# Performance work log

Hardware: AMD Instinct MI355X
Metric: run time of the kernel (lower is better)

## Reference

```python
import jax, jax.numpy as jnp
import numpy as np

N = 8192  # number of nodes
F = 8     # feature dim


def setup_inputs() -> dict:
    key = jax.random.key(0)
    ks = jax.random.split(key, 24)
    inp = {
        "adj": jax.random.uniform(ks[0], (N, N), jnp.float32),
        "dist_from_prev": jax.random.uniform(ks[1], (N,), jnp.float32),
        "dist_to_start": jax.random.uniform(ks[2], (N,), jnp.float32),
    }
    dims = {"l0": (2, F), "l1": (F, F), "pol": (F, 1), "val": (F, 1)}
    i = 3
    for name, (din, dout) in dims.items():
        inp[f"W1_{name}"] = jax.random.normal(ks[i], (din, dout), jnp.float32) * 0.3; i += 1
        inp[f"b1_{name}"] = jax.random.normal(ks[i], (dout,), jnp.float32) * 0.1; i += 1
        inp[f"W2_{name}"] = jax.random.normal(ks[i], (dout, dout), jnp.float32) * 0.3; i += 1
        inp[f"b2_{name}"] = jax.random.normal(ks[i], (dout,), jnp.float32) * 0.1; i += 1
    return inp


def _mlp(x, adj, W1, b1, W2, b2):
    # GIN-style layer: aggregate then 2-layer MLP
    h = adj @ x                     # [N, din] aggregation (memory bound)
    h = jax.nn.relu(h @ W1 + b1)    # [N, dout]
    return h @ W2 + b2              # [N, dout]


def reference(adj, dist_from_prev, dist_to_start,
              W1_l0, b1_l0, W2_l0, b2_l0,
              W1_l1, b1_l1, W2_l1, b2_l1,
              W1_pol, b1_pol, W2_pol, b2_pol,
              W1_val, b1_val, W2_val, b2_val):
    cur = jnp.stack([dist_from_prev, dist_to_start], axis=1)  # [N, 2]
    # hidden GIN layers + relu (dropout is identity in eval mode)
    cur = jax.nn.relu(_mlp(cur, adj, W1_l0, b1_l0, W2_l0, b2_l0))
    cur = jax.nn.relu(_mlp(cur, adj, W1_l1, b1_l1, W2_l1, b2_l1))
    policy = jax.nn.softmax(_mlp(cur, adj, W1_pol, b1_pol, W2_pol, b2_pol)[:, 0], axis=0)  # [N]
    value = _mlp(cur, adj, W1_val, b1_val, W2_val, b2_val)[:, 0]  # [N]
    m = value.mean()
    std = jnp.sqrt(jnp.mean((value - m) ** 2) + 1e-10)
    normalized_value = (value - m) / std
    return policy, normalized_value
```

## Files before the change

kernel.cpp:

```cpp
#include <hip/hip_runtime.h>
#include <math.h>

#define NN 8192
typedef unsigned int u32;

__device__ __forceinline__ u32 dot4u(u32 a, u32 b, u32 c) {
#if __has_builtin(__builtin_amdgcn_udot4)
  return __builtin_amdgcn_udot4(a, b, c, false);
#else
  c += (a & 0xffu) * (b & 0xffu);
  c += ((a >> 8) & 0xffu) * ((b >> 8) & 0xffu);
  c += ((a >> 16) & 0xffu) * ((b >> 16) & 0xffu);
  c += (a >> 24) * (b >> 24);
  return c;
#endif
}

__global__ __launch_bounds__(256, 8) void pass1_kernel(
    const float* __restrict__ adj, u32* __restrict__ adj8,
    const float* __restrict__ dfp, const float* __restrict__ dts,
    const float* __restrict__ W1, const float* __restrict__ b1,
    const float* __restrict__ W2, const float* __restrict__ b2,
    float* __restrict__ cur, float* __restrict__ partial,
    u32* __restrict__ cnt) {
  const int tid = threadIdx.x, wave = tid >> 6, lane = tid & 63;
  const int row = blockIdx.x * 4 + wave;
  __shared__ float wmax[4][8];
  if (blockIdx.x == 0 && tid == 0) cnt[0] = 0;

  const float* rowp = adj + (size_t)row * NN;
  u32* qp = adj8 + (size_t)row * 2048;

  float acc0 = 0.f, acc1 = 0.f;
  float4 A0 = *(const float4*)(rowp + 4 * lane);
  float4 A1 = *(const float4*)(rowp + 256 + 4 * lane);
  for (int c = 0; c < 16; ++c) {
    const int kb = 512 * c;
    float4 xp0 = *(const float4*)(dfp + kb + 4 * lane);
    float4 xp1 = *(const float4*)(dfp + kb + 256 + 4 * lane);
    float4 xs0 = *(const float4*)(dts + kb + 4 * lane);
    float4 xs1 = *(const float4*)(dts + kb + 256 + 4 * lane);
    float4 B0, B1;
    if (c < 15) {
      B0 = *(const float4*)(rowp + kb + 512 + 4 * lane);
      B1 = *(const float4*)(rowp + kb + 768 + 4 * lane);
    } else {
      B0 = A0; B1 = A1;
    }
    acc0 = fmaf(A0.x, xp0.x, acc0); acc0 = fmaf(A0.y, xp0.y, acc0);
    acc0 = fmaf(A0.z, xp0.z, acc0); acc0 = fmaf(A0.w, xp0.w, acc0);
    acc0 = fmaf(A1.x, xp1.x, acc0); acc0 = fmaf(A1.y, xp1.y, acc0);
    acc0 = fmaf(A1.z, xp1.z, acc0); acc0 = fmaf(A1.w, xp1.w, acc0);
    acc1 = fmaf(A0.x, xs0.x, acc1); acc1 = fmaf(A0.y, xs0.y, acc1);
    acc1 = fmaf(A0.z, xs0.z, acc1); acc1 = fmaf(A0.w, xs0.w, acc1);
    acc1 = fmaf(A1.x, xs1.x, acc1); acc1 = fmaf(A1.y, xs1.y, acc1);
    acc1 = fmaf(A1.z, xs1.z, acc1); acc1 = fmaf(A1.w, xs1.w, acc1);
    {
      u32 q0 = (u32)fmaf(A0.x, 255.f, 0.5f);
      u32 q1 = (u32)fmaf(A0.y, 255.f, 0.5f);
      u32 q2 = (u32)fmaf(A0.z, 255.f, 0.5f);
      u32 q3 = (u32)fmaf(A0.w, 255.f, 0.5f);
      qp[128 * c + lane] = q0 | (q1 << 8) | (q2 << 16) | (q3 << 24);
      q0 = (u32)fmaf(A1.x, 255.f, 0.5f);
      q1 = (u32)fmaf(A1.y, 255.f, 0.5f);
      q2 = (u32)fmaf(A1.z, 255.f, 0.5f);
      q3 = (u32)fmaf(A1.w, 255.f, 0.5f);
      qp[128 * c + 64 + lane] = q0 | (q1 << 8) | (q2 << 16) | (q3 << 24);
    }
    A0 = B0; A1 = B1;
  }
  for (int off = 32; off; off >>= 1) {
    acc0 += __shfl_xor(acc0, off, 64);
    acc1 += __shfl_xor(acc1, off, 64);
  }
  const int j = lane & 7;
  float z = fmaf(acc0, W1[j], fmaf(acc1, W1[8 + j], b1[j]));
  z = fmaxf(z, 0.f);
  float o = b2[j];
#pragma unroll
  for (int jj = 0; jj < 8; ++jj)
    o = fmaf(__shfl(z, jj, 64), W2[jj * 8 + j], o);
  float val = fmaxf(o, 0.f);
  if (lane < 8) {
    cur[(size_t)row * 8 + j] = val;
    wmax[wave][j] = val;
  }
  __syncthreads();
  if (tid < 8)
    partial[blockIdx.x * 8 + tid] = fmaxf(fmaxf(wmax[0][tid], wmax[1][tid]),
                                          fmaxf(wmax[2][tid], wmax[3][tid]));
}

template <int HEADS>
__global__ __launch_bounds__(512, 4) void pass23_kernel(
    const u32* __restrict__ adj8, const float* __restrict__ x,
    const float* __restrict__ partial, int nprod,
    const float* __restrict__ W1, const float* __restrict__ b1,
    const float* __restrict__ W2, const float* __restrict__ b2,
    const float* __restrict__ W1v, const float* __restrict__ b1v,
    const float* __restrict__ W2v, const float* __restrict__ b2v,
    float* __restrict__ out0, float* __restrict__ out1,
    float* __restrict__ partial_out, u32* __restrict__ cnt) {
  __shared__ u32 sxT[8 * 2048];
  __shared__ float redM[8][8];
  __shared__ float sqs[8], sds[8];
  __shared__ float wmax[8][8];
  __shared__ float sa[8], sb[8], sc[4];
  __shared__ int lastFlag;
  const int tid = threadIdx.x, wave = tid >> 6, lane = tid & 63;
  const int row0 = blockIdx.x * 16 + wave * 2;

  const u32* r0p = adj8 + (size_t)row0 * 2048;
  const u32* r1p = adj8 + (size_t)(row0 + 1) * 2048;
  uint4 A[2], Bp[2];
  A[0] = *(const uint4*)(r0p + 4 * lane);
  A[1] = *(const uint4*)(r1p + 4 * lane);
  Bp[0] = *(const uint4*)(r0p + 256 + 4 * lane);
  Bp[1] = *(const uint4*)(r1p + 256 + 4 * lane);

  float pm[8] = {0.f, 0.f, 0.f, 0.f, 0.f, 0.f, 0.f, 0.f};
  for (int p = tid; p < nprod; p += 512) {
    float4 a = *(const float4*)(partial + p * 8);
    float4 b = *(const float4*)(partial + p * 8 + 4);
    pm[0] = fmaxf(pm[0], a.x); pm[1] = fmaxf(pm[1], a.y);
    pm[2] = fmaxf(pm[2], a.z); pm[3] = fmaxf(pm[3], a.w);
    pm[4] = fmaxf(pm[4], b.x); pm[5] = fmaxf(pm[5], b.y);
    pm[6] = fmaxf(pm[6], b.z); pm[7] = fmaxf(pm[7], b.w);
  }
  for (int off = 32; off; off >>= 1)
#pragma unroll
    for (int j = 0; j < 8; ++j) pm[j] = fmaxf(pm[j], __shfl_xor(pm[j], off, 64));
  if (lane == 0)
#pragma unroll
    for (int j = 0; j < 8; ++j) redM[wave][j] = pm[j];
  __syncthreads();
  if (tid < 8) {
    float m2 = 0.f;
#pragma unroll
    for (int w = 0; w < 8; ++w) m2 = fmaxf(m2, redM[w][tid]);
    m2 = fmaxf(m2, 1e-20f);
    sqs[tid] = 255.f / m2;
    sds[tid] = m2 / 65025.f;
  }
  __syncthreads();

  float qs[8];
#pragma unroll
  for (int j = 0; j < 8; ++j) qs[j] = sqs[j];
  for (int gi = 0; gi < 4; ++gi) {
    const int p = gi * 512 + tid;
    u32 pk[8] = {0, 0, 0, 0, 0, 0, 0, 0};
#pragma unroll
    for (int m = 0; m < 4; ++m) {
      const float* xr = x + (size_t)(4 * p + m) * 8;
      float4 a = *(const float4*)xr;
      float4 b = *(const float4*)(xr + 4);
      const float e[8] = {a.x, a.y, a.z, a.w, b.x, b.y, b.z, b.w};
#pragma unroll
      for (int j = 0; j < 8; ++j)
        pk[j] |= ((u32)fmaf(e[j], qs[j], 0.5f)) << (8 * m);
    }
#pragma unroll
    for (int j = 0; j < 8; ++j) sxT[j * 2048 + p] = pk[j];
  }
  __syncthreads();

  u32 acc[2][8] = {};
  for (int c = 0; c < 8; ++c) {
    uint4 C[2];
    if (c + 2 < 8) {
      C[0] = *(const uint4*)(r0p + 256 * (c + 2) + 4 * lane);
      C[1] = *(const uint4*)(r1p + 256 * (c + 2) + 4 * lane);
    } else {
      C[0] = A[0];
      C[1] = A[1];
    }
    uint4 xq[8];
#pragma unroll
    for (int jj = 0; jj < 8; ++jj)
      xq[jj] = ((const uint4*)sxT)[jj * 512 + 64 * c + lane];
#pragma unroll
    for (int r = 0; r < 2; ++r) {
      const uint4 a4 = A[r];
#pragma unroll
      for (int jj = 0; jj < 8; ++jj) {
        u32 cc = acc[r][jj];
        cc = dot4u(a4.x, xq[jj].x, cc);
        cc = dot4u(a4.y, xq[jj].y, cc);
        cc = dot4u(a4.z, xq[jj].z, cc);
        cc = dot4u(a4.w, xq[jj].w, cc);
        acc[r][jj] = cc;
      }
    }
    A[0] = Bp[0]; A[1] = Bp[1];
    Bp[0] = C[0]; Bp[1] = C[1];
  }
#pragma unroll
  for (int r = 0; r < 2; ++r)
#pragma unroll
    for (int jj = 0; jj < 8; ++jj)
      for (int off = 32; off; off >>= 1)
        acc[r][jj] += (u32)__shfl_xor((int)acc[r][jj], off, 64);
  float h[2][8];
#pragma unroll
  for (int r = 0; r < 2; ++r)
#pragma unroll
    for (int jj = 0; jj < 8; ++jj) h[r][jj] = (float)acc[r][jj] * sds[jj];

  if (HEADS == 0) {
    const int j = lane & 7;
    float mxv = 0.f;
#pragma unroll
    for (int r = 0; r < 2; ++r) {
      float z = b1[j];
#pragma unroll
      for (int d = 0; d < 8; ++d) z = fmaf(h[r][d], W1[d * 8 + j], z);
      z = fmaxf(z, 0.f);
      float o = b2[j];
#pragma unroll
      for (int jj = 0; jj < 8; ++jj)
        o = fmaf(__shfl(z, jj, 64), W2[jj * 8 + j], o);
      float val = fmaxf(o, 0.f);
      if (lane < 8) out0[(size_t)(row0 + r) * 8 + j] = val;
      mxv = fmaxf(mxv, val);
    }
    if (lane < 8) wmax[wave][lane] = mxv;
    __syncthreads();
    if (tid < 8) {
      float m2 = 0.f;
#pragma unroll
      for (int w = 0; w < 8; ++w) m2 = fmaxf(m2, wmax[w][tid]);
      partial_out[blockIdx.x * 8 + tid] = m2;
    }
  } else {
    if (lane == 0) {
#pragma unroll
      for (int r = 0; r < 2; ++r) {
        float zp = b1[0], zv = b1v[0];
#pragma unroll
        for (int d = 0; d < 8; ++d) {
          zp = fmaf(h[r][d], W1[d], zp);
          zv = fmaf(h[r][d], W1v[d], zv);
        }
        zp = fmaxf(zp, 0.f);
        zv = fmaxf(zv, 0.f);
        out0[row0 + r] = fmaf(zp, W2[0], b2[0]);
        out1[row0 + r] = fmaf(zv, W2v[0], b2v[0]);
      }
    }
    __syncthreads();
    if (tid == 0) {
      __threadfence();
      u32 old = atomicAdd(cnt, 1);
      lastFlag = (old == (u32)(gridDim.x - 1)) ? 1 : 0;
    }
    __syncthreads();
    if (lastFlag) {
      __threadfence();
      float lv[16], vv[16];
#pragma unroll
      for (int i = 0; i < 4; ++i) {
        float4 a = *(const float4*)(out0 + tid * 16 + 4 * i);
        float4 b = *(const float4*)(out1 + tid * 16 + 4 * i);
        lv[4 * i] = a.x; lv[4 * i + 1] = a.y; lv[4 * i + 2] = a.z; lv[4 * i + 3] = a.w;
        vv[4 * i] = b.x; vv[4 * i + 1] = b.y; vv[4 * i + 2] = b.z; vv[4 * i + 3] = b.w;
      }
      float m = -3.4e38f, s = 0.f;
#pragma unroll
      for (int i = 0; i < 16; ++i) {
        m = fmaxf(m, lv[i]);
        s += vv[i];
      }
      for (int off = 32; off; off >>= 1) {
        m = fmaxf(m, __shfl_xor(m, off, 64));
        s += __shfl_xor(s, off, 64);
      }
      if (lane == 0) { sa[wave] = m; sb[wave] = s; }
      __syncthreads();
      if (tid == 0) {
        float mm = sa[0], ss = sb[0];
        for (int i = 1; i < 8; ++i) { mm = fmaxf(mm, sa[i]); ss += sb[i]; }
        sc[0] = mm; sc[1] = ss * (1.f / NN);
      }
      __syncthreads();
      m = sc[0];
      const float mean = sc[1];
      float e = 0.f, v2 = 0.f;
#pragma unroll
      for (int i = 0; i < 16; ++i) {
        e += expf(lv[i] - m);
        float d = vv[i] - mean;
        v2 = fmaf(d, d, v2);
      }
      for (int off = 32; off; off >>= 1) {
        e += __shfl_xor(e, off, 64);
        v2 += __shfl_xor(v2, off, 64);
      }
      if (lane == 0) { sa[wave] = e; sb[wave] = v2; }
      __syncthreads();
      if (tid == 0) {
        float ee = sa[0], vvv = sb[0];
        for (int i = 1; i < 8; ++i) { ee += sa[i]; vvv += sb[i]; }
        sc[2] = 1.f / ee;
        sc[3] = 1.f / sqrtf(vvv * (1.f / NN) + 1e-10f);
      }
      __syncthreads();
      const float inv_e = sc[2], inv_std = sc[3];
#pragma unroll
      for (int i = 0; i < 4; ++i) {
        float4 po, nv;
        po.x = expf(lv[4 * i] - m) * inv_e;
        po.y = expf(lv[4 * i + 1] - m) * inv_e;
        po.z = expf(lv[4 * i + 2] - m) * inv_e;
        po.w = expf(lv[4 * i + 3] - m) * inv_e;
        nv.x = (vv[4 * i] - mean) * inv_std;
        nv.y = (vv[4 * i + 1] - mean) * inv_std;
        nv.z = (vv[4 * i + 2] - mean) * inv_std;
        nv.w = (vv[4 * i + 3] - mean) * inv_std;
        *(float4*)(out0 + tid * 16 + 4 * i) = po;
        *(float4*)(out1 + tid * 16 + 4 * i) = nv;
      }
    }
  }
}

extern "C" void kernel_launch(void* const* d_in, const int* in_sizes, int n_in,
                              void* d_out, int out_size, void* d_ws,
                              size_t ws_size, hipStream_t stream) {
  const float* adj = (const float*)d_in[0];
  const float* dfp = (const float*)d_in[1];
  const float* dts = (const float*)d_in[2];
  const float* W1_l0 = (const float*)d_in[3];
  const float* b1_l0 = (const float*)d_in[4];
  const float* W2_l0 = (const float*)d_in[5];
  const float* b2_l0 = (const float*)d_in[6];
  const float* W1_l1 = (const float*)d_in[7];
  const float* b1_l1 = (const float*)d_in[8];
  const float* W2_l1 = (const float*)d_in[9];
  const float* b2_l1 = (const float*)d_in[10];
  const float* W1_pol = (const float*)d_in[11];
  const float* b1_pol = (const float*)d_in[12];
  const float* W2_pol = (const float*)d_in[13];
  const float* b2_pol = (const float*)d_in[14];
  const float* W1_val = (const float*)d_in[15];
  const float* b1_val = (const float*)d_in[16];
  const float* W2_val = (const float*)d_in[17];
  const float* b2_val = (const float*)d_in[18];

  char* base = (char*)d_ws;
  u32* adj8 = (u32*)base;
  float* curA = (float*)(base + (size_t)NN * NN);
  float* curB = curA + NN * 8;
  float* partialA = curB + NN * 8;
  float* partialB = partialA + 2048 * 8;
  u32* cnt = (u32*)(partialB + 512 * 8);
  float* logits = (float*)d_out;
  float* value = logits + NN;

  pass1_kernel<<<2048, 256, 0, stream>>>(adj, adj8, dfp, dts, W1_l0, b1_l0,
                                         W2_l0, b2_l0, curA, partialA, cnt);
  pass23_kernel<0><<<512, 512, 0, stream>>>(
      adj8, curA, partialA, 2048, W1_l1, b1_l1, W2_l1, b2_l1, W1_l1, b1_l1,
      W2_l1, b2_l1, curB, curB, partialB, cnt);
  pass23_kernel<1><<<512, 512, 0, stream>>>(
      adj8, curB, partialB, 512, W1_pol, b1_pol, W2_pol, b2_pol, W1_val,
      b1_val, W2_val, b2_val, logits, value, partialB, cnt);
}
```

Baseline: 151.4 us.

## Split quantization into streaming kernel and run layer-0 aggregation on uint8 adjacency

The fused first pass is split in two. A grid-stride kernel now only converts the fp32 adjacency to packed uint8, and a new layer-0 kernel reads that uint8 copy and does the aggregation with udot4 against quantized input features. The aim is a leaner streaming quantization pass and an integer aggregation that matches the later passes. In exchange it adds an extra 64 MB read of adj8 and one more launch, and quantizing the distance features to 8 bits adds numeric error.

```diff
diff --git a/kernel.cpp b/kernel.cpp
--- a/kernel.cpp
+++ b/kernel.cpp
@@ -16,79 +16,117 @@
 #endif
 }
 
-__global__ __launch_bounds__(256, 8) void pass1_kernel(
-    const float* __restrict__ adj, u32* __restrict__ adj8,
-    const float* __restrict__ dfp, const float* __restrict__ dts,
-    const float* __restrict__ W1, const float* __restrict__ b1,
-    const float* __restrict__ W2, const float* __restrict__ b2,
-    float* __restrict__ cur, float* __restrict__ partial,
+__device__ __forceinline__ u32 pack255(float4 v) {
+  u32 q0 = (u32)fmaf(v.x, 255.f, 0.5f);
+  u32 q1 = (u32)fmaf(v.y, 255.f, 0.5f);
+  u32 q2 = (u32)fmaf(v.z, 255.f, 0.5f);
+  u32 q3 = (u32)fmaf(v.w, 255.f, 0.5f);
+  return q0 | (q1 << 8) | (q2 << 16) | (q3 << 24);
+}
+
+__global__ __launch_bounds__(256) void quant_kernel(
+    const float4* __restrict__ adj4, u32* __restrict__ adj8,
     u32* __restrict__ cnt) {
+  if (blockIdx.x == 0 && threadIdx.x == 0) cnt[0] = 0;
+  const size_t n4 = (size_t)NN * NN / 4;
+  const size_t stride = (size_t)gridDim.x * 256;
+  for (size_t i = (size_t)blockIdx.x * 256 + threadIdx.x; i < n4;
+       i += 4 * stride) {
+    float4 v0 = adj4[i];
+    float4 v1 = adj4[i + stride];
+    float4 v2 = adj4[i + 2 * stride];
+    float4 v3 = adj4[i + 3 * stride];
+    adj8[i] = pack255(v0);
+    adj8[i + stride] = pack255(v1);
+    adj8[i + 2 * stride] = pack255(v2);
+    adj8[i + 3 * stride] = pack255(v3);
+  }
+}
+
+__global__ __launch_bounds__(512, 4) void agg0_kernel(
+    const u32* __restrict__ adj8, const float* __restrict__ dfp,
+    const float* __restrict__ dts, const float* __restrict__ W1,
+    const float* __restrict__ b1, const float* __restrict__ W2,
+    const float* __restrict__ b2, float* __restrict__ cur,
+    float* __restrict__ partial) {
+  __shared__ u32 sxT[2 * 2048];
+  __shared__ float wmax[8][8];
   const int tid = threadIdx.x, wave = tid >> 6, lane = tid & 63;
-  const int row = blockIdx.x * 4 + wave;
-  __shared__ float wmax[4][8];
-  if (blockIdx.x == 0 && tid == 0) cnt[0] = 0;
-
-  const float* rowp = adj + (size_t)row * NN;
-  u32* qp = adj8 + (size_t)row * 2048;
-
-  float acc0 = 0.f, acc1 = 0.f;
-  float4 A0 = *(const float4*)(rowp + 4 * lane);
-  float4 A1 = *(const float4*)(rowp + 256 + 4 * lane);
-  for (int c = 0; c < 16; ++c) {
-    const int kb = 512 * c;
-    float4 xp0 = *(const float4*)(dfp + kb + 4 * lane);
-    float4 xp1 = *(const float4*)(dfp + kb + 256 + 4 * lane);
-    float4 xs0 = *(const float4*)(dts + kb + 4 * lane);
-    float4 xs1 = *(const float4*)(dts + kb + 256 + 4 * lane);
-    float4 B0, B1;
-    if (c < 15) {
-      B0 = *(const float4*)(rowp + kb + 512 + 4 * lane);
-      B1 = *(const float4*)(rowp + kb + 768 + 4 * lane);
+  const int row0 = blockIdx.x * 16 + wave * 2;
+  const u32* r0p = adj8 + (size_t)row0 * 2048;
+  const u32* r1p = adj8 + (size_t)(row0 + 1) * 2048;
+
+  uint4 A[2], Bp[2];
+  A[0] = *(const uint4*)(r0p + 4 * lane);
+  A[1] = *(const uint4*)(r1p + 4 * lane);
+  Bp[0] = *(const uint4*)(r0p + 256 + 4 * lane);
+  Bp[1] = *(const uint4*)(r1p + 256 + 4 * lane);
+
+  for (int gi = 0; gi < 4; ++gi) {
+    const int p = gi * 512 + tid;
+    float4 a = *(const float4*)(dfp + 4 * p);
+    float4 b = *(const float4*)(dts + 4 * p);
+    sxT[p] = pack255(a);
+    sxT[2048 + p] = pack255(b);
+  }
+  __syncthreads();
+
+  u32 acc[2][2] = {};
+  for (int c = 0; c < 8; ++c) {
+    uint4 C[2];
+    if (c + 2 < 8) {
+      C[0] = *(const uint4*)(r0p + 256 * (c + 2) + 4 * lane);
+      C[1] = *(const uint4*)(r1p + 256 * (c + 2) + 4 * lane);
     } else {
-      B0 = A0; B1 = A1;
-    }
-    acc0 = fmaf(A0.x, xp0.x, acc0); acc0 = fmaf(A0.y, xp0.y, acc0);
-    acc0 = fmaf(A0.z, xp0.z, acc0); acc0 = fmaf(A0.w, xp0.w, acc0);
-    acc0 = fmaf(A1.x, xp1.x, acc0); acc0 = fmaf(A1.y, xp1.y, acc0);
-    acc0 = fmaf(A1.z, xp1.z, acc0); acc0 = fmaf(A1.w, xp1.w, acc0);
-    acc1 = fmaf(A0.x, xs0.x, acc1); acc1 = fmaf(A0.y, xs0.y, acc1);
-    acc1 = fmaf(A0.z, xs0.z, acc1); acc1 = fmaf(A0.w, xs0.w, acc1);
-    acc1 = fmaf(A1.x, xs1.x, acc1); acc1 = fmaf(A1.y, xs1.y, acc1);
-    acc1 = fmaf(A1.z, xs1.z, acc1); acc1 = fmaf(A1.w, xs1.w, acc1);
-    {
-      u32 q0 = (u32)fmaf(A0.x, 255.f, 0.5f);
-      u32 q1 = (u32)fmaf(A0.y, 255.f, 0.5f);
-      u32 q2 = (u32)fmaf(A0.z, 255.f, 0.5f);
-      u32 q3 = (u32)fmaf(A0.w, 255.f, 0.5f);
-      qp[128 * c + lane] = q0 | (q1 << 8) | (q2 << 16) | (q3 << 24);
-      q0 = (u32)fmaf(A1.x, 255.f, 0.5f);
-      q1 = (u32)fmaf(A1.y, 255.f, 0.5f);
-      q2 = (u32)fmaf(A1.z, 255.f, 0.5f);
-      q3 = (u32)fmaf(A1.w, 255.f, 0.5f);
-      qp[128 * c + 64 + lane] = q0 | (q1 << 8) | (q2 << 16) | (q3 << 24);
-    }
-    A0 = B0; A1 = B1;
-  }
-  for (int off = 32; off; off >>= 1) {
-    acc0 += __shfl_xor(acc0, off, 64);
-    acc1 += __shfl_xor(acc1, off, 64);
-  }
+      C[0] = A[0];
+      C[1] = A[1];
+    }
+    uint4 x0 = ((const uint4*)sxT)[64 * c + lane];
+    uint4 x1 = ((const uint4*)sxT)[512 + 64 * c + lane];
+#pragma unroll
+    for (int r = 0; r < 2; ++r) {
+      const uint4 a4 = A[r];
+      u32 c0 = acc[r][0], c1 = acc[r][1];
+      c0 = dot4u(a4.x, x0.x, c0); c0 = dot4u(a4.y, x0.y, c0);
+      c0 = dot4u(a4.z, x0.z, c0); c0 = dot4u(a4.w, x0.w, c0);
+      c1 = dot4u(a4.x, x1.x, c1); c1 = dot4u(a4.y, x1.y, c1);
+      c1 = dot4u(a4.z, x1.z, c1); c1 = dot4u(a4.w, x1.w, c1);
+      acc[r][0] = c0; acc[r][1] = c1;
+    }
+    A[0] = Bp[0]; A[1] = Bp[1];
+    Bp[0] = C[0]; Bp[1] = C[1];
+  }
+#pragma unroll
+  for (int r = 0; r < 2; ++r)
+#pragma unroll
+    for (int f = 0; f < 2; ++f)
+      for (int off = 32; off; off >>= 1)
+        acc[r][f] += (u32)__shfl_xor((int)acc[r][f], off, 64);
+
+  const float ds = 1.f / 65025.f;
   const int j = lane & 7;
-  float z = fmaf(acc0, W1[j], fmaf(acc1, W1[8 + j], b1[j]));
-  z = fmaxf(z, 0.f);
-  float o = b2[j];
-#pragma unroll
-  for (int jj = 0; jj < 8; ++jj)
-    o = fmaf(__shfl(z, jj, 64), W2[jj * 8 + j], o);
-  float val = fmaxf(o, 0.f);
-  if (lane < 8) {
-    cur[(size_t)row * 8 + j] = val;
-    wmax[wave][j] = val;
-  }
+  float mxv = 0.f;
+#pragma unroll
+  for (int r = 0; r < 2; ++r) {
+    float hp = (float)acc[r][0] * ds, hs = (float)acc[r][1] * ds;
+    float z = fmaf(hp, W1[j], fmaf(hs, W1[8 + j], b1[j]));
+    z = fmaxf(z, 0.f);
+    float o = b2[j];
+#pragma unroll
+    for (int jj = 0; jj < 8; ++jj)
+      o = fmaf(__shfl(z, jj, 64), W2[jj * 8 + j], o);
+    float val = fmaxf(o, 0.f);
+    if (lane < 8) cur[(size_t)(row0 + r) * 8 + j] = val;
+    mxv = fmaxf(mxv, val);
+  }
+  if (lane < 8) wmax[wave][lane] = mxv;
   __syncthreads();
-  if (tid < 8)
-    partial[blockIdx.x * 8 + tid] = fmaxf(fmaxf(wmax[0][tid], wmax[1][tid]),
-                                          fmaxf(wmax[2][tid], wmax[3][tid]));
+  if (tid < 8) {
+    float m2 = 0.f;
+#pragma unroll
+    for (int w = 0; w < 8; ++w) m2 = fmaxf(m2, wmax[w][tid]);
+    partial[blockIdx.x * 8 + tid] = m2;
+  }
 }
 
 template <int HEADS>
@@ -352,15 +390,16 @@
   float* curA = (float*)(base + (size_t)NN * NN);
   float* curB = curA + NN * 8;
   float* partialA = curB + NN * 8;
-  float* partialB = partialA + 2048 * 8;
+  float* partialB = partialA + 512 * 8;
   u32* cnt = (u32*)(partialB + 512 * 8);
   float* logits = (float*)d_out;
   float* value = logits + NN;
 
-  pass1_kernel<<<2048, 256, 0, stream>>>(adj, adj8, dfp, dts, W1_l0, b1_l0,
-                                         W2_l0, b2_l0, curA, partialA, cnt);
+  quant_kernel<<<2048, 256, 0, stream>>>((const float4*)adj, adj8, cnt);
+  agg0_kernel<<<512, 512, 0, stream>>>(adj8, dfp, dts, W1_l0, b1_l0, W2_l0,
+                                       b2_l0, curA, partialA);
   pass23_kernel<0><<<512, 512, 0, stream>>>(
-      adj8, curA, partialA, 2048, W1_l1, b1_l1, W2_l1, b2_l1, W1_l1, b1_l1,
+      adj8, curA, partialA, 512, W1_l1, b1_l1, W2_l1, b2_l1, W1_l1, b1_l1,
       W2_l1, b2_l1, curB, curB, partialB, cnt);
   pass23_kernel<1><<<512, 512, 0, stream>>>(
       adj8, curB, partialB, 512, W1_pol, b1_pol, W2_pol, b2_pol, W1_val,
```

Result: slower. 155.7 us (+2.8%).
